# Kernel tuning notes

Hardware: AMD Instinct MI355X
Metric: run time of the kernel (lower is better)

## Reference

```python
import jax, jax.numpy as jnp
import numpy as np

BN_EPS = 1e-5


def setup_inputs() -> dict:
    key = jax.random.key(0)
    k1, k2 = jax.random.split(key)
    bs, planes, h, w = 16, 64, 256, 256
    x = jax.random.normal(k1, (bs, planes, h, w), dtype=jnp.float32)
    # kaiming_normal_ on (planes, h, h): fan_in = h*h, std = sqrt(2/fan_in)
    std = np.sqrt(2.0 / (h * h)).astype(np.float32)
    weights = jax.random.normal(k2, (planes, h, h), dtype=jnp.float32) * std
    gamma = jnp.ones((planes,), dtype=jnp.float32)
    beta = jnp.zeros((planes,), dtype=jnp.float32)
    return {"x": x, "weights": weights, "gamma": gamma, "beta": beta}


def reference(x, weights, gamma, beta):
    bs, planes, h, w = x.shape
    xf = x.reshape(bs * planes, h, w)
    # batched Gram matrix: [bs*planes, h, h]
    g = jnp.einsum('nij,nkj->nik', xf, xf)
    g = jnp.triu(g)                              # keep upper triangle (incl. diag)
    g = g.reshape(bs, planes, h, h) * weights[None]  # per-plane elementwise weight
    # BatchNorm2d (training mode): biased batch stats over (N, H, W) per channel
    mean = jnp.mean(g, axis=(0, 2, 3), keepdims=True)
    var = jnp.mean(jnp.square(g - mean), axis=(0, 2, 3), keepdims=True)
    g_hat = (g - mean) * jax.lax.rsqrt(var + BN_EPS)
    out = g_hat * gamma[None, :, None, None] + beta[None, :, None, None]
    return out
```

## Files before the change

### kernel.cpp

```cpp
#include <hip/hip_runtime.h>

#define HD 256
#define NCH 64
#define NB 16
#define NPLANE (NB * NCH)
#define NPC (NB * HD * HD)
#define PLANE_ELEMS (HD * HD)

typedef __attribute__((ext_vector_type(4))) float f32x4;
typedef __attribute__((ext_vector_type(8))) short s16x8;
typedef __attribute__((ext_vector_type(4))) short s16x4;

__device__ __forceinline__ short f2bf(float f) {
    unsigned u = __float_as_uint(f);
    u += 0x7FFFu + ((u >> 16) & 1u);
    return (short)(u >> 16);
}

__device__ __forceinline__ void gl2lds16(const void* g, void* l) {
    __builtin_amdgcn_global_load_lds(
        (const __attribute__((address_space(1))) unsigned int*)g,
        (__attribute__((address_space(3))) unsigned int*)l, 16, 0, 0);
}

__global__ __launch_bounds__(256) void convert_kernel(
    const float* __restrict__ x, short* __restrict__ xb)
{
    size_t i = ((size_t)blockIdx.x * 256 + threadIdx.x) * 8;
    f32x4 a = *(const f32x4*)&x[i];
    f32x4 b = *(const f32x4*)&x[i + 4];
    s16x8 o = { f2bf(a.x), f2bf(a.y), f2bf(a.z), f2bf(a.w),
                f2bf(b.x), f2bf(b.y), f2bf(b.z), f2bf(b.w) };
    *(s16x8*)&xb[i] = o;
}

__global__ __launch_bounds__(256) void gram_kernel(
    const short* __restrict__ xb, const float* __restrict__ w,
    float* __restrict__ out, float* __restrict__ stats)
{
    const int tile = blockIdx.x;
    const int b    = blockIdx.y;
    const int c    = blockIdx.z;
    const int n    = b * NCH + c;
    const int tid  = threadIdx.x;

    const int ti = (tile == 2) ? 1 : 0;
    const int tk = (tile == 0) ? 0 : 1;
    const bool diag = (ti == tk);

    __shared__ short As[4096];
    __shared__ short Bs[4096];
    __shared__ float red[512];

    const short* xpA = xb + (size_t)n * PLANE_ELEMS + (size_t)ti * 128 * HD;
    const short* xpB = xb + (size_t)n * PLANE_ELEMS + (size_t)tk * 128 * HD;

    const int wid   = tid >> 6;
    const int lane  = tid & 63;
    const int waveM = wid >> 1, waveN = wid & 1;
    const int lrow  = lane & 15;
    const int q     = lane >> 4;

    f32x4 acc[4][4];
    for (int i = 0; i < 4; ++i)
        for (int j = 0; j < 4; ++j)
            acc[i][j] = (f32x4){0.f, 0.f, 0.f, 0.f};

    const int ch0 = tid;
    const int ch1 = tid + 256;
    const int q0 = ch0 >> 7, r0 = ch0 & 127;
    const int q1 = ch1 >> 7, r1 = ch1 & 127;

    for (int kb = 0; kb < 8; ++kb) {
        const int kbase = kb * 32;
        gl2lds16(xpA + (size_t)r0 * HD + kbase + q0 * 8, &As[(ch0 & ~63) * 8]);
        gl2lds16(xpA + (size_t)r1 * HD + kbase + q1 * 8, &As[(ch1 & ~63) * 8]);
        if (!diag) {
            gl2lds16(xpB + (size_t)r0 * HD + kbase + q0 * 8, &Bs[(ch0 & ~63) * 8]);
            gl2lds16(xpB + (size_t)r1 * HD + kbase + q1 * 8, &Bs[(ch1 & ~63) * 8]);
        }
        __syncthreads();

        s16x8 af[4], bfr[4];
        for (int mi = 0; mi < 4; ++mi) {
            int row = waveM * 64 + mi * 16 + lrow;
            af[mi] = *(s16x8*)&As[(q * 128 + row) * 8];
        }
        const short* Bsrc = diag ? As : Bs;
        for (int ni = 0; ni < 4; ++ni) {
            int row = waveN * 64 + ni * 16 + lrow;
            bfr[ni] = *(s16x8*)&Bsrc[(q * 128 + row) * 8];
        }
        for (int mi = 0; mi < 4; ++mi)
            for (int ni = 0; ni < 4; ++ni)
                acc[mi][ni] = __builtin_amdgcn_mfma_f32_16x16x32_bf16(
                    af[mi], bfr[ni], acc[mi][ni], 0, 0, 0);
        __syncthreads();
    }

    float lsum = 0.f, lsq = 0.f;
    const int row0 = (lane >> 4) * 4;
    const int col0 = lane & 15;
    for (int mi = 0; mi < 4; ++mi) {
        for (int ni = 0; ni < 4; ++ni) {
            int gk = tk * 128 + waveN * 64 + ni * 16 + col0;
            for (int r = 0; r < 4; ++r) {
                int gi = ti * 128 + waveM * 64 + mi * 16 + row0 + r;
                float v = acc[mi][ni][r];
                float val = (gk >= gi)
                    ? v * w[(size_t)c * PLANE_ELEMS + (size_t)gi * HD + gk]
                    : 0.f;
                lsum += val;
                lsq  += val * val;
                out[(size_t)n * PLANE_ELEMS + (size_t)gi * HD + gk] = val;
            }
        }
    }

    red[tid]       = lsum;
    red[256 + tid] = lsq;
    __syncthreads();
    for (int s = 128; s > 0; s >>= 1) {
        if (tid < s) {
            red[tid]       += red[tid + s];
            red[256 + tid] += red[256 + tid + s];
        }
        __syncthreads();
    }
    if (tid == 0) {
        atomicAdd(&stats[2*c],     red[0]);
        atomicAdd(&stats[2*c + 1], red[256]);
    }
}

__global__ __launch_bounds__(256) void bn_kernel(
    const float* __restrict__ gamma, const float* __restrict__ beta,
    float* __restrict__ out, const float* __restrict__ stats)
{
    const int n   = blockIdx.x;
    const int seg = blockIdx.y;
    const int tid = threadIdx.x;
    const int c   = n & (NCH - 1);

    float s  = stats[2*c];
    float sq = stats[2*c + 1];
    float mean = s * (1.0f / (float)NPC);
    float var  = sq * (1.0f / (float)NPC) - mean * mean;
    float rstd = rsqrtf(var + 1e-5f);
    float scale = rstd * gamma[c];
    float shift = beta[c] - mean * scale;

    float* op = out + (size_t)n * PLANE_ELEMS;
    f32x4 cv = {shift, shift, shift, shift};
    for (int k = 0; k < 4; ++k) {
        int f4 = seg * 1024 + k * 256 + tid;
        int r  = f4 >> 6;
        int c4 = f4 & 63;
        if (r >= 128 && c4 < 32) {
            *(f32x4*)&op[(size_t)f4 * 4] = cv;
        } else {
            f32x4 v = *(const f32x4*)&op[(size_t)f4 * 4];
            v.x = v.x * scale + shift;
            v.y = v.y * scale + shift;
            v.z = v.z * scale + shift;
            v.w = v.w * scale + shift;
            *(f32x4*)&op[(size_t)f4 * 4] = v;
        }
    }
}

template <int PASS>
__global__ __launch_bounds__(256) void gram_bn_fb(
    const float* __restrict__ x, const float* __restrict__ w,
    const float* __restrict__ gamma, const float* __restrict__ beta,
    float* __restrict__ out, float* __restrict__ stats)
{
    const int tile = blockIdx.x;
    const int b    = blockIdx.y;
    const int c    = blockIdx.z;
    const int n    = b * NCH + c;
    const int tid  = threadIdx.x;

    float mean = 0.f, rstd = 0.f, gm = 0.f, bt = 0.f;
    if (PASS == 1) {
        float s  = stats[2*c];
        float sq = stats[2*c+1];
        mean = s * (1.0f / (float)NPC);
        float var = sq * (1.0f / (float)NPC) - mean * mean;
        rstd = rsqrtf(var + 1e-5f);
        gm = gamma[c]; bt = beta[c];
    }
    if (PASS == 1 && tile == 3) {
        float v = (0.f - mean) * rstd * gm + bt;
        f32x4 vv = {v, v, v, v};
        float* op = out + (size_t)n * PLANE_ELEMS;
        for (int it = 0; it < 16; ++it) {
            int t  = it * 256 + tid;
            int r  = t >> 5;
            int c4 = (t & 31) * 4;
            *(f32x4*)&op[(size_t)(128 + r) * HD + c4] = vv;
        }
        return;
    }
    int ti, tk;
    if      (tile == 0) { ti = 0; tk = 0; }
    else if (tile == 1) { ti = 0; tk = 1; }
    else                { ti = 1; tk = 1; }
    const float* xp = x + (size_t)n * PLANE_ELEMS;
    __shared__ short As[128 * 40];
    __shared__ short Bs[128 * 40];
    __shared__ float red[512];
    const int wid   = tid >> 6;
    const int lane  = tid & 63;
    const int waveM = wid >> 1, waveN = wid & 1;
    const int lrow  = lane & 15;
    const int lkk   = (lane >> 4) * 8;
    f32x4 acc[4][4];
    for (int i = 0; i < 4; ++i)
        for (int j = 0; j < 4; ++j)
            acc[i][j] = (f32x4){0.f, 0.f, 0.f, 0.f};
    const int rr = tid >> 3;
    const int cc = (tid & 7) * 4;
    for (int kb = 0; kb < 8; ++kb) {
        for (int it = 0; it < 4; ++it) {
            int r = rr + it * 32;
            f32x4 av = *(const f32x4*)&xp[(size_t)(ti*128 + r) * HD + kb*32 + cc];
            f32x4 bv = *(const f32x4*)&xp[(size_t)(tk*128 + r) * HD + kb*32 + cc];
            s16x4 a4 = { f2bf(av.x), f2bf(av.y), f2bf(av.z), f2bf(av.w) };
            s16x4 b4 = { f2bf(bv.x), f2bf(bv.y), f2bf(bv.z), f2bf(bv.w) };
            *(s16x4*)&As[r*40 + cc] = a4;
            *(s16x4*)&Bs[r*40 + cc] = b4;
        }
        __syncthreads();
        s16x8 af[4], bfr[4];
        for (int mi = 0; mi < 4; ++mi)
            af[mi]  = *(s16x8*)&As[(waveM*64 + mi*16 + lrow)*40 + lkk];
        for (int ni = 0; ni < 4; ++ni)
            bfr[ni] = *(s16x8*)&Bs[(waveN*64 + ni*16 + lrow)*40 + lkk];
        for (int mi = 0; mi < 4; ++mi)
            for (int ni = 0; ni < 4; ++ni)
                acc[mi][ni] = __builtin_amdgcn_mfma_f32_16x16x32_bf16(
                    af[mi], bfr[ni], acc[mi][ni], 0, 0, 0);
        __syncthreads();
    }
    float lsum = 0.f, lsq = 0.f;
    const int row0 = (lane >> 4) * 4;
    const int col0 = lane & 15;
    for (int mi = 0; mi < 4; ++mi) {
        for (int ni = 0; ni < 4; ++ni) {
            int gk = tk*128 + waveN*64 + ni*16 + col0;
            for (int r = 0; r < 4; ++r) {
                int gi = ti*128 + waveM*64 + mi*16 + row0 + r;
                float v = acc[mi][ni][r];
                float val = (gk >= gi)
                    ? v * w[(size_t)c * PLANE_ELEMS + (size_t)gi * HD + gk]
                    : 0.f;
                if (PASS == 0) { lsum += val; lsq += val * val; }
                else out[(size_t)n * PLANE_ELEMS + (size_t)gi * HD + gk] =
                        (val - mean) * rstd * gm + bt;
            }
        }
    }
    if (PASS == 0) {
        red[tid] = lsum; red[256 + tid] = lsq;
        __syncthreads();
        for (int s = 128; s > 0; s >>= 1) {
            if (tid < s) { red[tid] += red[tid+s]; red[256+tid] += red[256+tid+s]; }
            __syncthreads();
        }
        if (tid == 0) {
            atomicAdd(&stats[2*c],     red[0]);
            atomicAdd(&stats[2*c + 1], red[256]);
        }
    }
}

extern "C" void kernel_launch(void* const* d_in, const int* in_sizes, int n_in,
                              void* d_out, int out_size, void* d_ws, size_t ws_size,
                              hipStream_t stream) {
    const float* x     = (const float*)d_in[0];
    const float* w     = (const float*)d_in[1];
    const float* gamma = (const float*)d_in[2];
    const float* beta  = (const float*)d_in[3];
    float* out   = (float*)d_out;
    float* stats = (float*)d_ws;

    hipMemsetAsync(d_ws, 0, 128 * sizeof(float), stream);

    const size_t xb_bytes = (size_t)NPLANE * PLANE_ELEMS * sizeof(short);
    if (ws_size >= 1024 + xb_bytes) {
        short* xb = (short*)((char*)d_ws + 1024);
        convert_kernel<<<dim3(32768), dim3(256), 0, stream>>>(x, xb);
        gram_kernel<<<dim3(3, NB, NCH), dim3(256), 0, stream>>>(xb, w, out, stats);
        bn_kernel<<<dim3(NPLANE, 16), dim3(256), 0, stream>>>(gamma, beta, out, stats);
    } else {
        gram_bn_fb<0><<<dim3(3, NB, NCH), dim3(256), 0, stream>>>(x, w, gamma, beta, out, stats);
        gram_bn_fb<1><<<dim3(4, NB, NCH), dim3(256), 0, stream>>>(x, w, gamma, beta, out, stats);
    }
}
```

Baseline: 706.0 us.

## Fuse bf16 conversion into per-plane Gram kernel and store bf16 intermediate

Removes the separate fp32-to-bf16 conversion pass: each block now handles a whole plane, loads fp32 rows, converts them in registers and writes them into a swizzled double-buffered LDS tile, prefetching the next k-chunk. The intermediate weighted Gram values go to a bf16 workspace instead of fp32 output, and the BN kernel reads these bf16 values and writes the constant for fully-lower-triangular chunks. This cuts global traffic (no xb round trip, half-size intermediate) at the cost of extra rounding of the pre-BN values and larger blocks with more LDS use.

Measured after the change: 614.2 us. 1.15x faster.

```diff
diff --git a/kernel.cpp b/kernel.cpp
--- a/kernel.cpp
+++ b/kernel.cpp
@@ -16,155 +16,205 @@
     u += 0x7FFFu + ((u >> 16) & 1u);
     return (short)(u >> 16);
 }
-
-__device__ __forceinline__ void gl2lds16(const void* g, void* l) {
-    __builtin_amdgcn_global_load_lds(
-        (const __attribute__((address_space(1))) unsigned int*)g,
-        (__attribute__((address_space(3))) unsigned int*)l, 16, 0, 0);
-}
-
-__global__ __launch_bounds__(256) void convert_kernel(
-    const float* __restrict__ x, short* __restrict__ xb)
+__device__ __forceinline__ float bf2f(short s) {
+    return __uint_as_float(((unsigned)(unsigned short)s) << 16);
+}
+
+__device__ __forceinline__ s16x8 ldfrag(const short* B, int row, int q) {
+    return *(const s16x8*)&B[row * 64 + ((q ^ (row & 7)) << 3)];
+}
+
+__global__ __launch_bounds__(512, 2) void gram_kernel(
+    const float* __restrict__ x, const float* __restrict__ w,
+    short* __restrict__ raw, float* __restrict__ stats)
 {
-    size_t i = ((size_t)blockIdx.x * 256 + threadIdx.x) * 8;
-    f32x4 a = *(const f32x4*)&x[i];
-    f32x4 b = *(const f32x4*)&x[i + 4];
-    s16x8 o = { f2bf(a.x), f2bf(a.y), f2bf(a.z), f2bf(a.w),
-                f2bf(b.x), f2bf(b.y), f2bf(b.z), f2bf(b.w) };
-    *(s16x8*)&xb[i] = o;
-}
-
-__global__ __launch_bounds__(256) void gram_kernel(
-    const short* __restrict__ xb, const float* __restrict__ w,
-    float* __restrict__ out, float* __restrict__ stats)
-{
-    const int tile = blockIdx.x;
-    const int b    = blockIdx.y;
-    const int c    = blockIdx.z;
-    const int n    = b * NCH + c;
+    const int n    = blockIdx.x;
+    const int c    = n & (NCH - 1);
     const int tid  = threadIdx.x;
-
-    const int ti = (tile == 2) ? 1 : 0;
-    const int tk = (tile == 0) ? 0 : 1;
-    const bool diag = (ti == tk);
-
-    __shared__ short As[4096];
-    __shared__ short Bs[4096];
-    __shared__ float red[512];
-
-    const short* xpA = xb + (size_t)n * PLANE_ELEMS + (size_t)ti * 128 * HD;
-    const short* xpB = xb + (size_t)n * PLANE_ELEMS + (size_t)tk * 128 * HD;
-
-    const int wid   = tid >> 6;
-    const int lane  = tid & 63;
-    const int waveM = wid >> 1, waveN = wid & 1;
+    const int wid  = tid >> 6;
+    const int lane = tid & 63;
+    const int waveM = wid >> 2;
+    const int waveN = wid & 3;
     const int lrow  = lane & 15;
-    const int q     = lane >> 4;
-
-    f32x4 acc[4][4];
-    for (int i = 0; i < 4; ++i)
-        for (int j = 0; j < 4; ++j)
-            acc[i][j] = (f32x4){0.f, 0.f, 0.f, 0.f};
-
-    const int ch0 = tid;
-    const int ch1 = tid + 256;
-    const int q0 = ch0 >> 7, r0 = ch0 & 127;
-    const int q1 = ch1 >> 7, r1 = ch1 & 127;
-
-    for (int kb = 0; kb < 8; ++kb) {
-        const int kbase = kb * 32;
-        gl2lds16(xpA + (size_t)r0 * HD + kbase + q0 * 8, &As[(ch0 & ~63) * 8]);
-        gl2lds16(xpA + (size_t)r1 * HD + kbase + q1 * 8, &As[(ch1 & ~63) * 8]);
-        if (!diag) {
-            gl2lds16(xpB + (size_t)r0 * HD + kbase + q0 * 8, &Bs[(ch0 & ~63) * 8]);
-            gl2lds16(xpB + (size_t)r1 * HD + kbase + q1 * 8, &Bs[(ch1 & ~63) * 8]);
-        }
+    const int qlane = lane >> 4;
+
+    __shared__ short As[2][16384];
+    __shared__ float redS[8], redQ[8];
+
+    const float* xp = x + (size_t)n * PLANE_ELEMS;
+    const int rs = tid >> 3;
+    const int qs = tid & 7;
+
+    f32x4 accA[4][4], accB[4][2];
+    #pragma unroll
+    for (int i = 0; i < 4; ++i) {
+        #pragma unroll
+        for (int j = 0; j < 4; ++j) accA[i][j] = (f32x4){0.f, 0.f, 0.f, 0.f};
+        accB[i][0] = (f32x4){0.f, 0.f, 0.f, 0.f};
+        accB[i][1] = (f32x4){0.f, 0.f, 0.f, 0.f};
+    }
+
+    f32x4 lr[4][2];
+
+    #pragma unroll
+    for (int j = 0; j < 4; ++j) {
+        const float* p = xp + (size_t)(j * 64 + rs) * HD + qs * 8;
+        lr[j][0] = *(const f32x4*)p;
+        lr[j][1] = *(const f32x4*)(p + 4);
+    }
+    #pragma unroll
+    for (int j = 0; j < 4; ++j) {
+        const int row = j * 64 + rs;
+        s16x8 o = { f2bf(lr[j][0].x), f2bf(lr[j][0].y), f2bf(lr[j][0].z), f2bf(lr[j][0].w),
+                    f2bf(lr[j][1].x), f2bf(lr[j][1].y), f2bf(lr[j][1].z), f2bf(lr[j][1].w) };
+        *(s16x8*)&As[0][row * 64 + ((qs ^ (row & 7)) << 3)] = o;
+    }
+
+    #pragma unroll
+    for (int kc = 0; kc < 4; ++kc) {
         __syncthreads();
-
-        s16x8 af[4], bfr[4];
-        for (int mi = 0; mi < 4; ++mi) {
-            int row = waveM * 64 + mi * 16 + lrow;
-            af[mi] = *(s16x8*)&As[(q * 128 + row) * 8];
-        }
-        const short* Bsrc = diag ? As : Bs;
+        if (kc < 3) {
+            #pragma unroll
+            for (int j = 0; j < 4; ++j) {
+                const float* p = xp + (size_t)(j * 64 + rs) * HD + (kc + 1) * 64 + qs * 8;
+                lr[j][0] = *(const f32x4*)p;
+                lr[j][1] = *(const f32x4*)(p + 4);
+            }
+        }
+        const short* B = As[kc & 1];
+        #pragma unroll
+        for (int kk = 0; kk < 2; ++kk) {
+            const int q = kk * 4 + qlane;
+            s16x8 a0[4], b0[4];
+            #pragma unroll
+            for (int mi = 0; mi < 4; ++mi)
+                a0[mi] = ldfrag(B, waveM * 64 + mi * 16 + lrow, q);
+            #pragma unroll
+            for (int ni = 0; ni < 4; ++ni)
+                b0[ni] = ldfrag(B, waveN * 64 + ni * 16 + lrow, q);
+            #pragma unroll
+            for (int mi = 0; mi < 4; ++mi)
+                #pragma unroll
+                for (int ni = 0; ni < 4; ++ni)
+                    accA[mi][ni] = __builtin_amdgcn_mfma_f32_16x16x32_bf16(
+                        a0[mi], b0[ni], accA[mi][ni], 0, 0, 0);
+            s16x8 a1[4], b1[2];
+            #pragma unroll
+            for (int mi = 0; mi < 4; ++mi)
+                a1[mi] = ldfrag(B, 128 + waveM * 64 + mi * 16 + lrow, q);
+            #pragma unroll
+            for (int ni = 0; ni < 2; ++ni)
+                b1[ni] = ldfrag(B, 128 + waveN * 32 + ni * 16 + lrow, q);
+            #pragma unroll
+            for (int mi = 0; mi < 4; ++mi)
+                #pragma unroll
+                for (int ni = 0; ni < 2; ++ni)
+                    accB[mi][ni] = __builtin_amdgcn_mfma_f32_16x16x32_bf16(
+                        a1[mi], b1[ni], accB[mi][ni], 0, 0, 0);
+        }
+        if (kc < 3) {
+            #pragma unroll
+            for (int j = 0; j < 4; ++j) {
+                const int row = j * 64 + rs;
+                s16x8 o = { f2bf(lr[j][0].x), f2bf(lr[j][0].y), f2bf(lr[j][0].z), f2bf(lr[j][0].w),
+                            f2bf(lr[j][1].x), f2bf(lr[j][1].y), f2bf(lr[j][1].z), f2bf(lr[j][1].w) };
+                *(s16x8*)&As[(kc + 1) & 1][row * 64 + ((qs ^ (row & 7)) << 3)] = o;
+            }
+        }
+    }
+
+    const float* wp = w + (size_t)c * PLANE_ELEMS;
+    short* rp = raw + (size_t)n * PLANE_ELEMS;
+    float lsum = 0.f, lsq = 0.f;
+    const int row0 = qlane * 4;
+    const int col0 = lrow;
+    #pragma unroll
+    for (int mi = 0; mi < 4; ++mi) {
+        #pragma unroll
         for (int ni = 0; ni < 4; ++ni) {
-            int row = waveN * 64 + ni * 16 + lrow;
-            bfr[ni] = *(s16x8*)&Bsrc[(q * 128 + row) * 8];
-        }
-        for (int mi = 0; mi < 4; ++mi)
-            for (int ni = 0; ni < 4; ++ni)
-                acc[mi][ni] = __builtin_amdgcn_mfma_f32_16x16x32_bf16(
-                    af[mi], bfr[ni], acc[mi][ni], 0, 0, 0);
-        __syncthreads();
-    }
-
-    float lsum = 0.f, lsq = 0.f;
-    const int row0 = (lane >> 4) * 4;
-    const int col0 = lane & 15;
-    for (int mi = 0; mi < 4; ++mi) {
-        for (int ni = 0; ni < 4; ++ni) {
-            int gk = tk * 128 + waveN * 64 + ni * 16 + col0;
+            const int gk = waveN * 64 + ni * 16 + col0;
+            #pragma unroll
             for (int r = 0; r < 4; ++r) {
-                int gi = ti * 128 + waveM * 64 + mi * 16 + row0 + r;
-                float v = acc[mi][ni][r];
-                float val = (gk >= gi)
-                    ? v * w[(size_t)c * PLANE_ELEMS + (size_t)gi * HD + gk]
-                    : 0.f;
+                const int gi = waveM * 64 + mi * 16 + row0 + r;
+                float v = accA[mi][ni][r];
+                float val = (gk >= gi) ? v * wp[gi * HD + gk] : 0.f;
                 lsum += val;
                 lsq  += val * val;
-                out[(size_t)n * PLANE_ELEMS + (size_t)gi * HD + gk] = val;
-            }
-        }
-    }
-
-    red[tid]       = lsum;
-    red[256 + tid] = lsq;
+                rp[gi * HD + gk] = f2bf(val);
+            }
+        }
+        #pragma unroll
+        for (int ni = 0; ni < 2; ++ni) {
+            const int gk = 128 + waveN * 32 + ni * 16 + col0;
+            #pragma unroll
+            for (int r = 0; r < 4; ++r) {
+                const int gi = 128 + waveM * 64 + mi * 16 + row0 + r;
+                float v = accB[mi][ni][r];
+                float val = (gk >= gi) ? v * wp[gi * HD + gk] : 0.f;
+                lsum += val;
+                lsq  += val * val;
+                rp[gi * HD + gk] = f2bf(val);
+            }
+        }
+    }
+
+    #pragma unroll
+    for (int off = 32; off > 0; off >>= 1) {
+        lsum += __shfl_down(lsum, off);
+        lsq  += __shfl_down(lsq, off);
+    }
+    if (lane == 0) { redS[wid] = lsum; redQ[wid] = lsq; }
     __syncthreads();
-    for (int s = 128; s > 0; s >>= 1) {
-        if (tid < s) {
-            red[tid]       += red[tid + s];
-            red[256 + tid] += red[256 + tid + s];
-        }
-        __syncthreads();
-    }
     if (tid == 0) {
-        atomicAdd(&stats[2*c],     red[0]);
-        atomicAdd(&stats[2*c + 1], red[256]);
+        float s = 0.f, s2 = 0.f;
+        #pragma unroll
+        for (int i = 0; i < 8; ++i) { s += redS[i]; s2 += redQ[i]; }
+        atomicAdd(&stats[2 * c],     s);
+        atomicAdd(&stats[2 * c + 1], s2);
     }
 }
 
 __global__ __launch_bounds__(256) void bn_kernel(
     const float* __restrict__ gamma, const float* __restrict__ beta,
-    float* __restrict__ out, const float* __restrict__ stats)
+    float* __restrict__ out, const float* __restrict__ stats,
+    const short* __restrict__ raw)
 {
     const int n   = blockIdx.x;
     const int seg = blockIdx.y;
     const int tid = threadIdx.x;
     const int c   = n & (NCH - 1);
 
-    float s  = stats[2*c];
-    float sq = stats[2*c + 1];
+    float s  = stats[2 * c];
+    float sq = stats[2 * c + 1];
     float mean = s * (1.0f / (float)NPC);
     float var  = sq * (1.0f / (float)NPC) - mean * mean;
     float rstd = rsqrtf(var + 1e-5f);
     float scale = rstd * gamma[c];
     float shift = beta[c] - mean * scale;
 
+    const short* rp = raw + (size_t)n * PLANE_ELEMS;
     float* op = out + (size_t)n * PLANE_ELEMS;
     f32x4 cv = {shift, shift, shift, shift};
-    for (int k = 0; k < 4; ++k) {
-        int f4 = seg * 1024 + k * 256 + tid;
-        int r  = f4 >> 6;
-        int c4 = f4 & 63;
-        if (r >= 128 && c4 < 32) {
-            *(f32x4*)&op[(size_t)f4 * 4] = cv;
+
+    #pragma unroll
+    for (int k = 0; k < 2; ++k) {
+        const int idx8 = seg * 512 + k * 256 + tid;
+        const int r  = idx8 >> 5;
+        const int c8 = idx8 & 31;
+        const bool cst = (r < 128) ? ((c8 * 8 + 7) < r)
+                                   : (c8 < 16 || (((c8 - 16) * 8 + 7) < (r - 128)));
+        float* o = &op[(size_t)idx8 * 8];
+        if (cst) {
+            *(f32x4*)o       = cv;
+            *(f32x4*)(o + 4) = cv;
         } else {
-            f32x4 v = *(const f32x4*)&op[(size_t)f4 * 4];
-            v.x = v.x * scale + shift;
-            v.y = v.y * scale + shift;
-            v.z = v.z * scale + shift;
-            v.w = v.w * scale + shift;
-            *(f32x4*)&op[(size_t)f4 * 4] = v;
+            s16x8 v = *(const s16x8*)&rp[(size_t)idx8 * 8];
+            f32x4 lo = { bf2f(v[0]) * scale + shift, bf2f(v[1]) * scale + shift,
+                         bf2f(v[2]) * scale + shift, bf2f(v[3]) * scale + shift };
+            f32x4 hi = { bf2f(v[4]) * scale + shift, bf2f(v[5]) * scale + shift,
+                         bf2f(v[6]) * scale + shift, bf2f(v[7]) * scale + shift };
+            *(f32x4*)o       = lo;
+            *(f32x4*)(o + 4) = hi;
         }
     }
 }
@@ -287,12 +337,11 @@
 
     hipMemsetAsync(d_ws, 0, 128 * sizeof(float), stream);
 
-    const size_t xb_bytes = (size_t)NPLANE * PLANE_ELEMS * sizeof(short);
-    if (ws_size >= 1024 + xb_bytes) {
-        short* xb = (short*)((char*)d_ws + 1024);
-        convert_kernel<<<dim3(32768), dim3(256), 0, stream>>>(x, xb);
-        gram_kernel<<<dim3(3, NB, NCH), dim3(256), 0, stream>>>(xb, w, out, stats);
-        bn_kernel<<<dim3(NPLANE, 16), dim3(256), 0, stream>>>(gamma, beta, out, stats);
+    const size_t raw_bytes = (size_t)NPLANE * PLANE_ELEMS * sizeof(short);
+    if (ws_size >= 1024 + raw_bytes) {
+        short* raw = (short*)((char*)d_ws + 1024);
+        gram_kernel<<<dim3(NPLANE), dim3(512), 0, stream>>>(x, w, raw, stats);
+        bn_kernel<<<dim3(NPLANE, 16), dim3(256), 0, stream>>>(gamma, beta, out, stats, raw);
     } else {
         gram_bn_fb<0><<<dim3(3, NB, NCH), dim3(256), 0, stream>>>(x, w, gamma, beta, out, stats);
         gram_bn_fb<1><<<dim3(4, NB, NCH), dim3(256), 0, stream>>>(x, w, gamma, beta, out, stats);
```
